# Optimization experiments

Hardware: AMD Instinct MI355X
Metric: run time of the kernel (lower is better)

Reference implementation:

```python
import jax, jax.numpy as jnp
import numpy as np

MAX_DEPTH = 10
NUM_INPUT = 256
NUM_OUTPUT = 64
BATCH = 131072
N_INTERNAL = 2**MAX_DEPTH - 1  # 1023 heap-indexed internal nodes
N_LEAVES = 2**MAX_DEPTH        # 1024 leaves


def setup_inputs() -> dict:
    key = jax.random.key(0)
    k_x, k_w, k_b, k_a, k_l = jax.random.split(key, 5)
    x = jax.random.normal(k_x, (BATCH, NUM_INPUT), dtype=jnp.float32)
    # internal-node params (torch init: weights ~ N(0,0.1); bias/alpha zeros,
    # but we randomize bias/alpha so both branches are exercised)
    W = jax.random.normal(k_w, (N_INTERNAL, NUM_INPUT), dtype=jnp.float32) * 0.1
    b = jax.random.normal(k_b, (N_INTERNAL,), dtype=jnp.float32) * 0.1
    alpha = jax.random.normal(k_a, (N_INTERNAL,), dtype=jnp.float32)
    leaves = jax.random.normal(k_l, (N_LEAVES, NUM_OUTPUT), dtype=jnp.float32)
    return {"x": x, "W": W, "b": b, "alpha": alpha, "leaves": leaves}


def reference(x, W, b, alpha, leaves):
    # Batched hard root-to-leaf traversal of the soft binary tree.
    # Heap indexing: node i -> left child 2i+1, right child 2i+2.
    B = x.shape[0]
    idx = jnp.zeros((B,), dtype=jnp.int32)
    mult = jnp.ones((B,), dtype=x.dtype)
    for _ in range(MAX_DEPTH):  # fixed small structural loop over depth levels
        w = W[idx]  # [B, F] gather of per-node weights
        val = jax.nn.sigmoid(alpha[idx] * (jnp.einsum('bf,bf->b', x, w) + b[idx]))
        go_right = val >= 0.5
        # right branch contributes val, left branch contributes (1 - val)
        mult = mult * jnp.where(go_right, val, 1.0 - val)
        idx = 2 * idx + 1 + go_right.astype(jnp.int32)
    leaf_idx = idx - N_INTERNAL  # [B]
    return mult[:, None] * leaves[leaf_idx]  # [B, num_output]
```

## Files before the change

### kernel.cpp

```cpp
#include <hip/hip_runtime.h>

#define NUM_INPUT   256
#define NUM_OUTPUT  64
#define MAX_DEPTH   10
#define N_INTERNAL  1023
#define STAGED_NODES 63
#define STAGED_DEPTH 6
#define ELEMS_PER_WAVE 4
#define WAVES_PER_BLOCK 16
#define THREADS (WAVES_PER_BLOCK * 64)
#define ELEMS_PER_BLOCK (WAVES_PER_BLOCK * ELEMS_PER_WAVE)

__global__ __launch_bounds__(THREADS) void ogtree_kernel(
    const float* __restrict__ x,
    const float* __restrict__ W,
    const float* __restrict__ b,
    const float* __restrict__ alpha,
    const float* __restrict__ leaves,
    float* __restrict__ out)
{
    __shared__ float lds_w[STAGED_NODES * NUM_INPUT];
    __shared__ float lds_b[N_INTERNAL];
    __shared__ float lds_a[N_INTERNAL];

    const int tid = threadIdx.x;

    {
        const float4* Wv = reinterpret_cast<const float4*>(W);
        float4* lw4 = reinterpret_cast<float4*>(lds_w);
        #pragma unroll
        for (int i = tid; i < STAGED_NODES * NUM_INPUT / 4; i += THREADS)
            lw4[i] = Wv[i];
        for (int i = tid; i < N_INTERNAL; i += THREADS) {
            lds_b[i] = b[i];
            lds_a[i] = alpha[i];
        }
    }
    __syncthreads();

    const int lane = tid & 63;
    const int wid  = tid >> 6;
    const int g    = lane >> 4;
    const int s    = lane & 15;
    const int elem = blockIdx.x * ELEMS_PER_BLOCK + wid * ELEMS_PER_WAVE + g;

    const float4* xrow = reinterpret_cast<const float4*>(x + (size_t)elem * NUM_INPUT);
    float4 xv[4];
    #pragma unroll
    for (int k = 0; k < 4; ++k)
        xv[k] = xrow[k * 16 + s];

    int   idx  = 0;
    float mult = 1.0f;

    #pragma unroll
    for (int d = 0; d < STAGED_DEPTH; ++d) {
        const float4* wrow = reinterpret_cast<const float4*>(lds_w + idx * NUM_INPUT);
        float acc = 0.0f;
        #pragma unroll
        for (int k = 0; k < 4; ++k) {
            float4 wv = wrow[k * 16 + s];
            acc = fmaf(xv[k].x, wv.x, acc);
            acc = fmaf(xv[k].y, wv.y, acc);
            acc = fmaf(xv[k].z, wv.z, acc);
            acc = fmaf(xv[k].w, wv.w, acc);
        }
        #pragma unroll
        for (int m = 1; m <= 8; m <<= 1)
            acc += __shfl_xor(acc, m);
        float z   = lds_a[idx] * (acc + lds_b[idx]);
        float val = 1.0f / (1.0f + __expf(-z));
        bool  right = (val >= 0.5f);
        mult *= right ? val : (1.0f - val);
        idx = 2 * idx + 1 + (right ? 1 : 0);
    }

    #pragma unroll
    for (int d = STAGED_DEPTH; d < MAX_DEPTH; ++d) {
        const float4* wrow = reinterpret_cast<const float4*>(W + (size_t)idx * NUM_INPUT);
        float acc = 0.0f;
        #pragma unroll
        for (int k = 0; k < 4; ++k) {
            float4 wv = wrow[k * 16 + s];
            acc = fmaf(xv[k].x, wv.x, acc);
            acc = fmaf(xv[k].y, wv.y, acc);
            acc = fmaf(xv[k].z, wv.z, acc);
            acc = fmaf(xv[k].w, wv.w, acc);
        }
        #pragma unroll
        for (int m = 1; m <= 8; m <<= 1)
            acc += __shfl_xor(acc, m);
        float z   = lds_a[idx] * (acc + lds_b[idx]);
        float val = 1.0f / (1.0f + __expf(-z));
        bool  right = (val >= 0.5f);
        mult *= right ? val : (1.0f - val);
        idx = 2 * idx + 1 + (right ? 1 : 0);
    }

    const int leaf = idx - N_INTERNAL;
    const float4 lv = reinterpret_cast<const float4*>(
        leaves + (size_t)leaf * NUM_OUTPUT)[s];
    float4 o;
    o.x = mult * lv.x;
    o.y = mult * lv.y;
    o.z = mult * lv.z;
    o.w = mult * lv.w;
    reinterpret_cast<float4*>(out + (size_t)elem * NUM_OUTPUT)[s] = o;
}

extern "C" void kernel_launch(void* const* d_in, const int* in_sizes, int n_in,
                              void* d_out, int out_size, void* d_ws, size_t ws_size,
                              hipStream_t stream) {
    const float* x      = (const float*)d_in[0];
    const float* W      = (const float*)d_in[1];
    const float* b      = (const float*)d_in[2];
    const float* alpha  = (const float*)d_in[3];
    const float* leaves = (const float*)d_in[4];
    float* out = (float*)d_out;

    const int batch  = in_sizes[0] / NUM_INPUT;
    const int blocks = batch / ELEMS_PER_BLOCK;

    ogtree_kernel<<<blocks, THREADS, 0, stream>>>(x, W, b, alpha, leaves, out);
}
```

Measured before the change: 50.49 us.

## Use persistent blocks with multi-round loop and two elements per lane group

Result: slower. 61.53 us (+21.9%).

```diff
diff --git a/kernel.cpp b/kernel.cpp
--- a/kernel.cpp
+++ b/kernel.cpp
@@ -6,10 +6,11 @@
 #define N_INTERNAL  1023
 #define STAGED_NODES 63
 #define STAGED_DEPTH 6
-#define ELEMS_PER_WAVE 4
 #define WAVES_PER_BLOCK 16
 #define THREADS (WAVES_PER_BLOCK * 64)
-#define ELEMS_PER_BLOCK (WAVES_PER_BLOCK * ELEMS_PER_WAVE)
+#define BLOCKS 256
+#define ELEMS_PER_WAVE_TOTAL 32
+#define ROUNDS 4
 
 __global__ __launch_bounds__(THREADS) void ogtree_kernel(
     const float* __restrict__ x,
@@ -42,70 +43,78 @@
     const int wid  = tid >> 6;
     const int g    = lane >> 4;
     const int s    = lane & 15;
-    const int elem = blockIdx.x * ELEMS_PER_BLOCK + wid * ELEMS_PER_WAVE + g;
+    const int wave_base = (blockIdx.x * WAVES_PER_BLOCK + wid) * ELEMS_PER_WAVE_TOTAL;
 
-    const float4* xrow = reinterpret_cast<const float4*>(x + (size_t)elem * NUM_INPUT);
-    float4 xv[4];
-    #pragma unroll
-    for (int k = 0; k < 4; ++k)
-        xv[k] = xrow[k * 16 + s];
+    for (int r = 0; r < ROUNDS; ++r) {
+        const int elemA = wave_base + r * 8 + g;
+        const int elemB = elemA + 4;
 
-    int   idx  = 0;
-    float mult = 1.0f;
-
-    #pragma unroll
-    for (int d = 0; d < STAGED_DEPTH; ++d) {
-        const float4* wrow = reinterpret_cast<const float4*>(lds_w + idx * NUM_INPUT);
-        float acc = 0.0f;
+        const float4* xrA = reinterpret_cast<const float4*>(x + (size_t)elemA * NUM_INPUT);
+        const float4* xrB = reinterpret_cast<const float4*>(x + (size_t)elemB * NUM_INPUT);
+        float4 xa[4], xb[4];
         #pragma unroll
         for (int k = 0; k < 4; ++k) {
-            float4 wv = wrow[k * 16 + s];
-            acc = fmaf(xv[k].x, wv.x, acc);
-            acc = fmaf(xv[k].y, wv.y, acc);
-            acc = fmaf(xv[k].z, wv.z, acc);
-            acc = fmaf(xv[k].w, wv.w, acc);
+            xa[k] = xrA[k * 16 + s];
+            xb[k] = xrB[k * 16 + s];
         }
+
+        int   idxA = 0,   idxB = 0;
+        float multA = 1.f, multB = 1.f;
+
         #pragma unroll
-        for (int m = 1; m <= 8; m <<= 1)
-            acc += __shfl_xor(acc, m);
-        float z   = lds_a[idx] * (acc + lds_b[idx]);
-        float val = 1.0f / (1.0f + __expf(-z));
-        bool  right = (val >= 0.5f);
-        mult *= right ? val : (1.0f - val);
-        idx = 2 * idx + 1 + (right ? 1 : 0);
+        for (int d = 0; d < MAX_DEPTH; ++d) {
+            const float4* wrA;
+            const float4* wrB;
+            if (d < STAGED_DEPTH) {
+                wrA = reinterpret_cast<const float4*>(lds_w + idxA * NUM_INPUT);
+                wrB = reinterpret_cast<const float4*>(lds_w + idxB * NUM_INPUT);
+            } else {
+                wrA = reinterpret_cast<const float4*>(W + (size_t)idxA * NUM_INPUT);
+                wrB = reinterpret_cast<const float4*>(W + (size_t)idxB * NUM_INPUT);
+            }
+            float accA = 0.f, accB = 0.f;
+            #pragma unroll
+            for (int k = 0; k < 4; ++k) {
+                float4 wa = wrA[k * 16 + s];
+                float4 wb = wrB[k * 16 + s];
+                accA = fmaf(xa[k].x, wa.x, accA);
+                accA = fmaf(xa[k].y, wa.y, accA);
+                accA = fmaf(xa[k].z, wa.z, accA);
+                accA = fmaf(xa[k].w, wa.w, accA);
+                accB = fmaf(xb[k].x, wb.x, accB);
+                accB = fmaf(xb[k].y, wb.y, accB);
+                accB = fmaf(xb[k].z, wb.z, accB);
+                accB = fmaf(xb[k].w, wb.w, accB);
+            }
+            #pragma unroll
+            for (int m = 1; m <= 8; m <<= 1) {
+                accA += __shfl_xor(accA, m);
+                accB += __shfl_xor(accB, m);
+            }
+            float zA = lds_a[idxA] * (accA + lds_b[idxA]);
+            float zB = lds_a[idxB] * (accB + lds_b[idxB]);
+            float vA = 1.0f / (1.0f + __expf(-zA));
+            float vB = 1.0f / (1.0f + __expf(-zB));
+            bool  rA = vA >= 0.5f;
+            bool  rB = vB >= 0.5f;
+            multA *= rA ? vA : (1.0f - vA);
+            multB *= rB ? vB : (1.0f - vB);
+            idxA = 2 * idxA + 1 + (rA ? 1 : 0);
+            idxB = 2 * idxB + 1 + (rB ? 1 : 0);
+        }
+
+        const float4 lvA = reinterpret_cast<const float4*>(
+            leaves + (size_t)(idxA - N_INTERNAL) * NUM_OUTPUT)[s];
+        const float4 lvB = reinterpret_cast<const float4*>(
+            leaves + (size_t)(idxB - N_INTERNAL) * NUM_OUTPUT)[s];
+        float4 oA, oB;
+        oA.x = multA * lvA.x; oA.y = multA * lvA.y;
+        oA.z = multA * lvA.z; oA.w = multA * lvA.w;
+        oB.x = multB * lvB.x; oB.y = multB * lvB.y;
+        oB.z = multB * lvB.z; oB.w = multB * lvB.w;
+        reinterpret_cast<float4*>(out + (size_t)elemA * NUM_OUTPUT)[s] = oA;
+        reinterpret_cast<float4*>(out + (size_t)elemB * NUM_OUTPUT)[s] = oB;
     }
-
-    #pragma unroll
-    for (int d = STAGED_DEPTH; d < MAX_DEPTH; ++d) {
-        const float4* wrow = reinterpret_cast<const float4*>(W + (size_t)idx * NUM_INPUT);
-        float acc = 0.0f;
-        #pragma unroll
-        for (int k = 0; k < 4; ++k) {
-            float4 wv = wrow[k * 16 + s];
-            acc = fmaf(xv[k].x, wv.x, acc);
-            acc = fmaf(xv[k].y, wv.y, acc);
-            acc = fmaf(xv[k].z, wv.z, acc);
-            acc = fmaf(xv[k].w, wv.w, acc);
-        }
-        #pragma unroll
-        for (int m = 1; m <= 8; m <<= 1)
-            acc += __shfl_xor(acc, m);
-        float z   = lds_a[idx] * (acc + lds_b[idx]);
-        float val = 1.0f / (1.0f + __expf(-z));
-        bool  right = (val >= 0.5f);
-        mult *= right ? val : (1.0f - val);
-        idx = 2 * idx + 1 + (right ? 1 : 0);
-    }
-
-    const int leaf = idx - N_INTERNAL;
-    const float4 lv = reinterpret_cast<const float4*>(
-        leaves + (size_t)leaf * NUM_OUTPUT)[s];
-    float4 o;
-    o.x = mult * lv.x;
-    o.y = mult * lv.y;
-    o.z = mult * lv.z;
-    o.w = mult * lv.w;
-    reinterpret_cast<float4*>(out + (size_t)elem * NUM_OUTPUT)[s] = o;
 }
 
 extern "C" void kernel_launch(void* const* d_in, const int* in_sizes, int n_in,
@@ -118,8 +127,5 @@
     const float* leaves = (const float*)d_in[4];
     float* out = (float*)d_out;
 
-    const int batch  = in_sizes[0] / NUM_INPUT;
-    const int blocks = batch / ELEMS_PER_BLOCK;
-
-    ogtree_kernel<<<blocks, THREADS, 0, stream>>>(x, W, b, alpha, leaves, out);
+    ogtree_kernel<<<BLOCKS, THREADS, 0, stream>>>(x, W, b, alpha, leaves, out);
 }
```
